# Kernel optimization log

Measured on AMD Instinct MI355X. Metric: run time of the kernel, lower is better.

## Reference

```python
import jax, jax.numpy as jnp
import numpy as np

B = 1024
IN_H, IN_W = 128, 128
KH, KW = 10, 10
SH, SW = 5, 5
PH, PW = 2, 2
HP, WP = IN_H + 2 * PH, IN_W + 2 * PW          # padded dims: 132, 132
NKH = (IN_H - KH + 2 * PH) // SH + 1            # 25
NKW = (IN_W - KW + 2 * PW) // SW + 1            # 25
NK = NKH * NKW                                  # 625


def _build_weight_matrix(kernel_weights):
    """kernel_weights: [NK, KH, KW] -> sparse-structured dense [HP*WP, NK].
    Faithful to LocallyConnected2dV2._create_weight_matrix, vectorized."""
    i = jnp.arange(NK)
    start_i = (i // NKW) * SH                   # [NK]
    start_j = (i % NKW) * SW                    # [NK]
    # flat row index for each (kernel, k, l) tap in padded image
    rows = ((start_i[:, None, None] + jnp.arange(KH)[None, :, None]) * WP
            + start_j[:, None, None] + jnp.arange(KW)[None, None, :])  # [NK,KH,KW]
    rows = rows.reshape(NK, KH * KW)
    cols = i[:, None]                           # [NK,1] broadcasts over taps
    W = jnp.zeros((HP * WP, NK), dtype=kernel_weights.dtype)
    return W.at[rows, cols].set(kernel_weights.reshape(NK, KH * KW))


def setup_inputs() -> dict:
    key = jax.random.key(0)
    kx, kw, kb = jax.random.split(key, 3)
    x = jax.random.normal(kx, (B, IN_H, IN_W), dtype=jnp.float32)
    kernel_weights = jax.random.normal(kw, (NK, KH, KW), dtype=jnp.float32)
    W = _build_weight_matrix(kernel_weights)    # [HP*WP, NK]
    bias = jax.random.normal(kb, (NKH, NKW), dtype=jnp.float32)
    return {"x": x, "W": W, "bias": bias}


def reference(x, W, bias):
    # zero-pad spatial dims, flatten, dense GEMM against sparse-structured W
    xp = jnp.pad(x, ((0, 0), (PH, PH), (PW, PW)))          # [B,HP,WP]
    xf = xp.reshape(x.shape[0], HP * WP)                   # [B,HP*WP]
    out = xf @ W                                           # [B,NK]
    out = out.reshape(x.shape[0], NKH, NKW)
    return out + bias
```

## Files before the change

### kernel.cpp

```cpp
#include <hip/hip_runtime.h>

typedef _Float16 f16x2 __attribute__((ext_vector_type(2)));
typedef __fp16  fp16x2 __attribute__((ext_vector_type(2)));

constexpr int NKH  = 25, NKW = 25, NK = 625;
constexpr int WPAD = 132;
constexpr int IMGS = 10;
constexpr int NGRP = (1024 + IMGS - 1) / IMGS;
constexpr int ROW_U2 = 34;
constexpr int IMG_U2 = 342;
constexpr int WPT  = 160;

union U2H { unsigned int u; f16x2 h; fp16x2 p; };

__global__ void gather_wp(const float* __restrict__ W, _Float16* __restrict__ wgp) {
    int t = blockIdx.x * 256 + threadIdx.x;
    if (t >= NK * WPT) return;
    int k = t / WPT, rem = t % WPT;
    int di = rem >> 4, p = rem & 15;
    int ki = k / NKW, kj = k % NKW;
    int o = (5 * kj + 2) & 3;
    int j = p - o;
    float val = 0.f;
    if (j >= 0 && j < 10)
        val = W[(size_t)((ki * 5 + di) * WPAD + kj * 5 + j) * NK + k];
    wgp[t] = (_Float16)val;
}

__device__ __forceinline__ float dot2acc(unsigned int a, unsigned int b, float c) {
    U2H ua, ub; ua.u = a; ub.u = b;
#if __has_builtin(__builtin_amdgcn_fdot2)
    return __builtin_amdgcn_fdot2(ua.h, ub.h, c, false);
#else
    return c + (float)ua.h.x * (float)ub.h.x + (float)ua.h.y * (float)ub.h.y;
#endif
}

template <bool USE_WG>
__global__ __launch_bounds__(256, 4)
void lc2d_f16(const float* __restrict__ x, const _Float16* __restrict__ wgp,
              const float* __restrict__ Wfull,
              const float* __restrict__ bias, float* __restrict__ out) {
    __shared__ uint2 xs2[IMGS * IMG_U2];

    const int bid = blockIdx.x;
    const int ki  = bid % NKH;
    const int grp = bid / NKH;
    const int tid = threadIdx.x;

    const int r0 = ki * 5 - 2;
    for (int i = tid; i < IMGS * 340; i += 256) {
        const int im = i / 340, rem = i % 340;
        const int r = rem / 34, q = rem % 34;
        const int rg = r0 + r;
        const int b  = grp * IMGS + im;
        uint2 val = make_uint2(0u, 0u);
        if (q >= 1 && q <= 32 && rg >= 0 && b < 1024) {
            const float4 v = *reinterpret_cast<const float4*>(
                x + ((size_t)b << 14) + (rg << 7) + ((q - 1) << 2));
            U2H u0, u1;
            u0.p = __builtin_amdgcn_cvt_pkrtz(v.x, v.y);
            u1.p = __builtin_amdgcn_cvt_pkrtz(v.z, v.w);
            val.x = u0.u; val.y = u1.u;
        }
        xs2[im * IMG_U2 + r * ROW_U2 + q] = val;
    }

    const bool active = tid < IMGS * NKW;
    const int img = tid / NKW, kj = tid % NKW;
    const int k = ki * NKW + kj;
    unsigned int wv[80];
    float bval = 0.f;
    if (active) {
        if (USE_WG) {
            const uint4* wp = reinterpret_cast<const uint4*>(wgp + (size_t)k * WPT);
#pragma unroll
            for (int t4 = 0; t4 < 20; ++t4) {
                uint4 u = wp[t4];
                wv[4 * t4 + 0] = u.x; wv[4 * t4 + 1] = u.y;
                wv[4 * t4 + 2] = u.z; wv[4 * t4 + 3] = u.w;
            }
        } else {
            const int o = (5 * kj + 2) & 3;
#pragma unroll
            for (int di = 0; di < 10; ++di) {
#pragma unroll
                for (int m = 0; m < 8; ++m) {
                    float f0 = 0.f, f1 = 0.f;
                    int j0 = 2 * m - o, j1 = 2 * m + 1 - o;
                    if (j0 >= 0 && j0 < 10)
                        f0 = Wfull[(size_t)((ki * 5 + di) * WPAD + kj * 5 + j0) * NK + k];
                    if (j1 >= 0 && j1 < 10)
                        f1 = Wfull[(size_t)((ki * 5 + di) * WPAD + kj * 5 + j1) * NK + k];
                    U2H u; u.p = __builtin_amdgcn_cvt_pkrtz(f0, f1);
                    wv[di * 8 + m] = u.u;
                }
            }
        }
        bval = bias[k];
    }
    __syncthreads();

    if (!active) return;

    const int h0 = (5 * kj + 2) & ~3;
    const uint2* base = xs2 + img * IMG_U2 + (h0 >> 2);
    float acc = 0.f;
#pragma unroll
    for (int di = 0; di < 10; ++di) {
        const uint2 a0 = base[di * ROW_U2 + 0];
        const uint2 a1 = base[di * ROW_U2 + 1];
        const uint2 a2 = base[di * ROW_U2 + 2];
        const uint2 a3 = base[di * ROW_U2 + 3];
        const unsigned int* w8 = &wv[di * 8];
        acc = dot2acc(a0.x, w8[0], acc);
        acc = dot2acc(a0.y, w8[1], acc);
        acc = dot2acc(a1.x, w8[2], acc);
        acc = dot2acc(a1.y, w8[3], acc);
        acc = dot2acc(a2.x, w8[4], acc);
        acc = dot2acc(a2.y, w8[5], acc);
        acc = dot2acc(a3.x, w8[6], acc);
        acc = dot2acc(a3.y, w8[7], acc);
    }
    const int b = grp * IMGS + img;
    if (b < 1024)
        out[(size_t)b * NK + k] = acc + bval;
}

extern "C" void kernel_launch(void* const* d_in, const int* in_sizes, int n_in,
                              void* d_out, int out_size, void* d_ws, size_t ws_size,
                              hipStream_t stream) {
    const float* x    = (const float*)d_in[0];
    const float* W    = (const float*)d_in[1];
    const float* bias = (const float*)d_in[2];
    float* out = (float*)d_out;

    const dim3 grid(NKH * NGRP);
    if (ws_size >= (size_t)NK * WPT * sizeof(_Float16)) {
        _Float16* wgp = (_Float16*)d_ws;
        gather_wp<<<(NK * WPT + 255) / 256, 256, 0, stream>>>(W, wgp);
        lc2d_f16<true><<<grid, 256, 0, stream>>>(x, wgp, W, bias, out);
    } else {
        lc2d_f16<false><<<grid, 256, 0, stream>>>(x, nullptr, W, bias, out);
    }
}
```

Before: 140.0 us.

## Restructure to one image-half per block, avoiding overlapping row reloads

The kernel used to give each block one kernel row for ten images, so the ten input rows were re-staged for every kernel row (about a 2x overlap). Now each block takes one image and half of its output rows (a 1024x2 grid) and stages each half-image into shared memory once. Each thread loops over several output positions and streams the fp16 weights from global/L2 in two chunks instead of holding 80 registers. The change cuts redundant x reads and register pressure, at the cost of weights being re-read per image through cache and some threads idling on the second loop pass.

```diff
diff --git a/kernel.cpp b/kernel.cpp
--- a/kernel.cpp
+++ b/kernel.cpp
@@ -3,13 +3,9 @@
 typedef _Float16 f16x2 __attribute__((ext_vector_type(2)));
 typedef __fp16  fp16x2 __attribute__((ext_vector_type(2)));
 
-constexpr int NKH  = 25, NKW = 25, NK = 625;
-constexpr int WPAD = 132;
-constexpr int IMGS = 10;
-constexpr int NGRP = (1024 + IMGS - 1) / IMGS;
-constexpr int ROW_U2 = 34;
-constexpr int IMG_U2 = 342;
-constexpr int WPT  = 160;
+constexpr int NKW  = 25, NK = 625;
+constexpr int WPADR = 132;
+constexpr int WPT   = 160;
 
 union U2H { unsigned int u; f16x2 h; fp16x2 p; };
 
@@ -23,7 +19,7 @@
     int j = p - o;
     float val = 0.f;
     if (j >= 0 && j < 10)
-        val = W[(size_t)((ki * 5 + di) * WPAD + kj * 5 + j) * NK + k];
+        val = W[(size_t)((ki * 5 + di) * WPADR + kj * 5 + j) * NK + k];
     wgp[t] = (_Float16)val;
 }
 
@@ -38,93 +34,89 @@
 
 template <bool USE_WG>
 __global__ __launch_bounds__(256, 4)
-void lc2d_f16(const float* __restrict__ x, const _Float16* __restrict__ wgp,
+void lc2d_img(const float* __restrict__ x, const _Float16* __restrict__ wgp,
               const float* __restrict__ Wfull,
               const float* __restrict__ bias, float* __restrict__ out) {
-    __shared__ uint2 xs2[IMGS * IMG_U2];
+    __shared__ uint2 xs[70 * 34];
 
-    const int bid = blockIdx.x;
-    const int ki  = bid % NKH;
-    const int grp = bid / NKH;
-    const int tid = threadIdx.x;
+    const int b    = blockIdx.x;
+    const int half = blockIdx.y;
+    const int P0   = half ? 65 : 0;
+    const int NR   = half ? 65 : 70;
+    const int K0   = half ? 13 : 0;
+    const int NOUT = half ? 300 : 325;
+    const int tid  = threadIdx.x;
 
-    const int r0 = ki * 5 - 2;
-    for (int i = tid; i < IMGS * 340; i += 256) {
-        const int im = i / 340, rem = i % 340;
-        const int r = rem / 34, q = rem % 34;
-        const int rg = r0 + r;
-        const int b  = grp * IMGS + im;
+    for (int i = tid; i < NR * 2; i += 256)
+        xs[(i >> 1) * 34 + (i & 1) * 33] = make_uint2(0u, 0u);
+
+    const float* xb = x + ((size_t)b << 14);
+    for (int i = tid; i < NR * 32; i += 256) {
+        const int idx = i >> 5, q = (i & 31) + 1;
+        const int r = P0 + idx - 2;
         uint2 val = make_uint2(0u, 0u);
-        if (q >= 1 && q <= 32 && rg >= 0 && b < 1024) {
-            const float4 v = *reinterpret_cast<const float4*>(
-                x + ((size_t)b << 14) + (rg << 7) + ((q - 1) << 2));
+        if (r >= 0 && r < 128) {
+            const float4 v = *reinterpret_cast<const float4*>(xb + (r << 7) + ((q - 1) << 2));
             U2H u0, u1;
             u0.p = __builtin_amdgcn_cvt_pkrtz(v.x, v.y);
             u1.p = __builtin_amdgcn_cvt_pkrtz(v.z, v.w);
             val.x = u0.u; val.y = u1.u;
         }
-        xs2[im * IMG_U2 + r * ROW_U2 + q] = val;
-    }
-
-    const bool active = tid < IMGS * NKW;
-    const int img = tid / NKW, kj = tid % NKW;
-    const int k = ki * NKW + kj;
-    unsigned int wv[80];
-    float bval = 0.f;
-    if (active) {
-        if (USE_WG) {
-            const uint4* wp = reinterpret_cast<const uint4*>(wgp + (size_t)k * WPT);
-#pragma unroll
-            for (int t4 = 0; t4 < 20; ++t4) {
-                uint4 u = wp[t4];
-                wv[4 * t4 + 0] = u.x; wv[4 * t4 + 1] = u.y;
-                wv[4 * t4 + 2] = u.z; wv[4 * t4 + 3] = u.w;
-            }
-        } else {
-            const int o = (5 * kj + 2) & 3;
-#pragma unroll
-            for (int di = 0; di < 10; ++di) {
-#pragma unroll
-                for (int m = 0; m < 8; ++m) {
-                    float f0 = 0.f, f1 = 0.f;
-                    int j0 = 2 * m - o, j1 = 2 * m + 1 - o;
-                    if (j0 >= 0 && j0 < 10)
-                        f0 = Wfull[(size_t)((ki * 5 + di) * WPAD + kj * 5 + j0) * NK + k];
-                    if (j1 >= 0 && j1 < 10)
-                        f1 = Wfull[(size_t)((ki * 5 + di) * WPAD + kj * 5 + j1) * NK + k];
-                    U2H u; u.p = __builtin_amdgcn_cvt_pkrtz(f0, f1);
-                    wv[di * 8 + m] = u.u;
-                }
-            }
-        }
-        bval = bias[k];
+        xs[idx * 34 + q] = val;
     }
     __syncthreads();
 
-    if (!active) return;
+    const uint4* wgp16 = reinterpret_cast<const uint4*>(wgp);
 
-    const int h0 = (5 * kj + 2) & ~3;
-    const uint2* base = xs2 + img * IMG_U2 + (h0 >> 2);
-    float acc = 0.f;
+    for (int k_local = tid; k_local < NOUT; k_local += 256) {
+        const int k    = K0 * 25 + k_local;
+        const int ki_l = k_local / 25;
+        const int kj   = k_local - ki_l * 25;
+        const uint2* base = xs + ki_l * 5 * 34 + ((5 * kj + 2) >> 2);
+        float acc = bias[k];
 #pragma unroll
-    for (int di = 0; di < 10; ++di) {
-        const uint2 a0 = base[di * ROW_U2 + 0];
-        const uint2 a1 = base[di * ROW_U2 + 1];
-        const uint2 a2 = base[di * ROW_U2 + 2];
-        const uint2 a3 = base[di * ROW_U2 + 3];
-        const unsigned int* w8 = &wv[di * 8];
-        acc = dot2acc(a0.x, w8[0], acc);
-        acc = dot2acc(a0.y, w8[1], acc);
-        acc = dot2acc(a1.x, w8[2], acc);
-        acc = dot2acc(a1.y, w8[3], acc);
-        acc = dot2acc(a2.x, w8[4], acc);
-        acc = dot2acc(a2.y, w8[5], acc);
-        acc = dot2acc(a3.x, w8[6], acc);
-        acc = dot2acc(a3.y, w8[7], acc);
+        for (int c = 0; c < 2; ++c) {
+            uint4 wq[10];
+            if (USE_WG) {
+#pragma unroll
+                for (int j = 0; j < 10; ++j) wq[j] = wgp16[k * 20 + c * 10 + j];
+            } else {
+                const int o = (5 * kj + 2) & 3;
+#pragma unroll
+                for (int j = 0; j < 10; ++j) {
+                    const int di = c * 5 + (j >> 1);
+                    const int pb = (j & 1) * 8;
+                    unsigned int uu[4];
+#pragma unroll
+                    for (int m = 0; m < 4; ++m) {
+                        float f0 = 0.f, f1 = 0.f;
+                        const int j0 = pb + 2 * m - o, j1 = pb + 2 * m + 1 - o;
+                        const size_t rowb = (size_t)(((K0 + ki_l) * 5 + di) * WPADR + kj * 5);
+                        if (j0 >= 0 && j0 < 10) f0 = Wfull[(rowb + j0) * NK + k];
+                        if (j1 >= 0 && j1 < 10) f1 = Wfull[(rowb + j1) * NK + k];
+                        U2H u; u.p = __builtin_amdgcn_cvt_pkrtz(f0, f1);
+                        uu[m] = u.u;
+                    }
+                    wq[j] = make_uint4(uu[0], uu[1], uu[2], uu[3]);
+                }
+            }
+#pragma unroll
+            for (int d2 = 0; d2 < 5; ++d2) {
+                const uint2* rowp = base + (c * 5 + d2) * 34;
+                const uint2 a0 = rowp[0], a1 = rowp[1], a2 = rowp[2], a3 = rowp[3];
+                const uint4 wA = wq[d2 * 2], wB = wq[d2 * 2 + 1];
+                acc = dot2acc(a0.x, wA.x, acc);
+                acc = dot2acc(a0.y, wA.y, acc);
+                acc = dot2acc(a1.x, wA.z, acc);
+                acc = dot2acc(a1.y, wA.w, acc);
+                acc = dot2acc(a2.x, wB.x, acc);
+                acc = dot2acc(a2.y, wB.y, acc);
+                acc = dot2acc(a3.x, wB.z, acc);
+                acc = dot2acc(a3.y, wB.w, acc);
+            }
+        }
+        out[(size_t)b * NK + k] = acc;
     }
-    const int b = grp * IMGS + img;
-    if (b < 1024)
-        out[(size_t)b * NK + k] = acc + bval;
 }
 
 extern "C" void kernel_launch(void* const* d_in, const int* in_sizes, int n_in,
@@ -135,12 +127,12 @@
     const float* bias = (const float*)d_in[2];
     float* out = (float*)d_out;
 
-    const dim3 grid(NKH * NGRP);
+    const dim3 grid(1024, 2);
     if (ws_size >= (size_t)NK * WPT * sizeof(_Float16)) {
         _Float16* wgp = (_Float16*)d_ws;
         gather_wp<<<(NK * WPT + 255) / 256, 256, 0, stream>>>(W, wgp);
-        lc2d_f16<true><<<grid, 256, 0, stream>>>(x, wgp, W, bias, out);
+        lc2d_img<true><<<grid, 256, 0, stream>>>(x, wgp, W, bias, out);
     } else {
-        lc2d_f16<false><<<grid, 256, 0, stream>>>(x, nullptr, W, bias, out);
+        lc2d_img<false><<<grid, 256, 0, stream>>>(x, nullptr, W, bias, out);
     }
 }
```

New measurement: 135.4 us. 1.03x faster.
